# Optimization experiments

Hardware: AMD Instinct MI355X
Metric: run time of the kernel (lower is better)

The kernel has to match this reference:

```python
import jax, jax.numpy as jnp
import numpy as np

B, Q, K, H, V = 16, 128, 512, 256, 256


def setup_inputs() -> dict:
    key = jax.random.key(0)
    ks = jax.random.split(key, 7)
    return {
        "queries": jax.random.normal(ks[0], (B, Q, H), dtype=jnp.float32),
        "keys": jax.random.normal(ks[1], (B, K, H), dtype=jnp.float32),
        "values": jax.random.normal(ks[2], (B, K, V), dtype=jnp.float32),
        "Wq": jax.random.normal(ks[3], (H, H), dtype=jnp.float32) / np.sqrt(H),
        "Wk": jax.random.normal(ks[4], (H, H), dtype=jnp.float32) / np.sqrt(H),
        "Wv": jax.random.normal(ks[5], (H,), dtype=jnp.float32) / np.sqrt(H),
        "valid_lens": jax.random.randint(ks[6], (B,), 1, K + 1, dtype=jnp.int32),
    }


def reference(queries, keys, values, Wq, Wk, Wv, valid_lens):
    # Projections (no bias, matching nn.Linear(..., bias=False))
    q = jnp.einsum("bqd,hd->bqh", queries, Wq)  # W_q: weight is [out,in] in torch; symmetric here
    k = jnp.einsum("bkd,hd->bkh", keys, Wk)
    # Broadcast add -> tanh -> project to scalar score: [B, Q, K]
    features = jnp.tanh(q[:, :, None, :] + k[:, None, :, :])  # [B,Q,K,H]
    scores = jnp.einsum("bqkh,h->bqk", features, Wv)
    # masked_softmax: positions >= valid_len get -1e6 before softmax
    mask = jnp.arange(K)[None, None, :] < valid_lens[:, None, None]  # [B,1,K]
    scores = jnp.where(mask, scores, -1e6)
    attn = jax.nn.softmax(scores, axis=-1)
    # dropout in eval mode = identity
    return jnp.einsum("bqk,bkv->bqv", attn, values)
```

## Files before the change

### kernel.cpp

```cpp
#include <hip/hip_runtime.h>

#define BQ   16
#define QLEN 128
#define KLEN 512
#define HD   256
#define VD   256

typedef __bf16 bf16x8 __attribute__((ext_vector_type(8)));
typedef float  f32x4  __attribute__((ext_vector_type(4)));

static __device__ __forceinline__ float fexp2(float x) {
#if __has_builtin(__builtin_amdgcn_exp2f)
    return __builtin_amdgcn_exp2f(x);
#else
    return exp2f(x);
#endif
}
static __device__ __forceinline__ float frcp(float x) {
#if __has_builtin(__builtin_amdgcn_rcpf)
    return __builtin_amdgcn_rcpf(x);
#else
    return 1.0f / x;
#endif
}

#define EXP_SCALE 2.8853900817779268f

__global__ __launch_bounds__(256) void mfma_proj(
    const float* __restrict__ queries, const float* __restrict__ keys,
    const float* __restrict__ Wq, const float* __restrict__ Wk,
    const int* __restrict__ vlen,
    float* __restrict__ Eq, float* __restrict__ Ekt)
{
    __shared__ __bf16 Ahi_s[64][40];
    __shared__ __bf16 Alo_s[64][40];
    __shared__ __bf16 Whi_s[64][40];
    __shared__ __bf16 Wlo_s[64][40];

    const int t    = threadIdx.x;
    const int ln   = t & 63;
    const int w    = t >> 6;
    const int p    = ln & 15;
    const int quad = ln >> 4;
    const int bx = blockIdx.x, by = blockIdx.y;
    const bool isq = by < 32;
    const int row0 = by * 64;
    const int col0 = bx * 64;

    if (!isq) {
        const int kr0 = row0 - 2048;
        if ((kr0 & 511) >= vlen[kr0 >> 9]) return;
    }

    const float* Ag = isq ? (queries + (size_t)row0 * HD)
                          : (keys + (size_t)(row0 - 2048) * HD);
    const float* Wg = isq ? Wq : Wk;

    const int ar = t >> 2, ac = (t & 3) * 8;

    float4 pa0, pa1, pw0, pw1;
    {
        const float* ap = Ag + ar * HD + ac;
        pa0 = *(const float4*)ap;
        pa1 = *(const float4*)(ap + 4);
        const float* wp = Wg + (size_t)(col0 + ar) * HD + ac;
        pw0 = *(const float4*)wp;
        pw1 = *(const float4*)(wp + 4);
    }

    f32x4 acc[4] = {};

    for (int s = 0; s < 8; ++s) {
        __syncthreads();
        {
            float fa[8] = {pa0.x, pa0.y, pa0.z, pa0.w, pa1.x, pa1.y, pa1.z, pa1.w};
            float fw[8] = {pw0.x, pw0.y, pw0.z, pw0.w, pw1.x, pw1.y, pw1.z, pw1.w};
            bf16x8 ha, la, hw, lw;
            #pragma unroll
            for (int j = 0; j < 8; ++j) {
                __bf16 av = (__bf16)fa[j];
                ha[j] = av;
                la[j] = (__bf16)(fa[j] - (float)av);
                __bf16 wv = (__bf16)fw[j];
                hw[j] = wv;
                lw[j] = (__bf16)(fw[j] - (float)wv);
            }
            *(bf16x8*)&Ahi_s[ar][ac] = ha;
            *(bf16x8*)&Alo_s[ar][ac] = la;
            *(bf16x8*)&Whi_s[ar][ac] = hw;
            *(bf16x8*)&Wlo_s[ar][ac] = lw;
        }
        __syncthreads();
        if (s < 7) {
            const int kc = (s + 1) * 32;
            const float* ap = Ag + ar * HD + kc + ac;
            pa0 = *(const float4*)ap;
            pa1 = *(const float4*)(ap + 4);
            const float* wp = Wg + (size_t)(col0 + ar) * HD + kc + ac;
            pw0 = *(const float4*)wp;
            pw1 = *(const float4*)(wp + 4);
        }
        bf16x8 bh = *(const bf16x8*)&Whi_s[w * 16 + p][quad * 8];
        bf16x8 bl = *(const bf16x8*)&Wlo_s[w * 16 + p][quad * 8];
        #pragma unroll
        for (int mi = 0; mi < 4; ++mi) {
            bf16x8 ah = *(const bf16x8*)&Ahi_s[mi * 16 + p][quad * 8];
            bf16x8 al = *(const bf16x8*)&Alo_s[mi * 16 + p][quad * 8];
            acc[mi] = __builtin_amdgcn_mfma_f32_16x16x32_bf16(ah, bh, acc[mi], 0, 0, 0);
            acc[mi] = __builtin_amdgcn_mfma_f32_16x16x32_bf16(ah, bl, acc[mi], 0, 0, 0);
            acc[mi] = __builtin_amdgcn_mfma_f32_16x16x32_bf16(al, bh, acc[mi], 0, 0, 0);
        }
    }

    #pragma unroll
    for (int mi = 0; mi < 4; ++mi) {
        const int H  = col0 + w * 16 + p;
        const int rl = mi * 16 + quad * 4;
        float e0 = fexp2(acc[mi][0] * EXP_SCALE);
        float e1 = fexp2(acc[mi][1] * EXP_SCALE);
        float e2 = fexp2(acc[mi][2] * EXP_SCALE);
        float e3 = fexp2(acc[mi][3] * EXP_SCALE);
        if (isq) {
            float* dst = Eq + (size_t)(row0 + rl) * HD + H;
            dst[0] = e0; dst[HD] = e1; dst[2 * HD] = e2; dst[3 * HD] = e3;
        } else {
            const int kr = row0 - 2048 + rl;
            const int b = kr >> 9, k0 = kr & 511;
            float4 st; st.x = e0; st.y = e1; st.z = e2; st.w = e3;
            *(float4*)(Ekt + ((size_t)b * HD + H) * KLEN + k0) = st;
        }
    }
}

__global__ __launch_bounds__(256) void proj_exp_gemm(
    const float* __restrict__ Qin, const float* __restrict__ Kin,
    const float* __restrict__ Wq, const float* __restrict__ Wk,
    float* __restrict__ Eq, float* __restrict__ Ekt)
{
    __shared__ union {
        struct { float a[2][16][68]; float w[2][16][68]; } s;
        float tb[64][65];
    } sh;

    const int t  = threadIdx.x;
    const int tx = t & 15, ty = t >> 4;
    const int bx = blockIdx.x, by = blockIdx.y;
    const bool isq = by < 32;
    const int row0 = isq ? by * 64 : (by - 32) * 64;
    const float* A = isq ? Qin : Kin;
    const float* W = isq ? Wq : Wk;
    const int lrow = t >> 2, ld0 = (t & 3) * 4;
    const float* Ab = A + (row0 + lrow) * HD;
    const float* Wb = W + (bx * 64 + lrow) * HD;

    float4 av = *(const float4*)(Ab + ld0);
    float4 wv = *(const float4*)(Wb + ld0);
    sh.s.a[0][ld0 + 0][lrow] = av.x; sh.s.a[0][ld0 + 1][lrow] = av.y;
    sh.s.a[0][ld0 + 2][lrow] = av.z; sh.s.a[0][ld0 + 3][lrow] = av.w;
    sh.s.w[0][ld0 + 0][lrow] = wv.x; sh.s.w[0][ld0 + 1][lrow] = wv.y;
    sh.s.w[0][ld0 + 2][lrow] = wv.z; sh.s.w[0][ld0 + 3][lrow] = wv.w;

    float acc[4][4] = {};
    int p = 0;
    for (int kc = 0; kc < HD; kc += 16) {
        if (kc + 16 < HD) {
            av = *(const float4*)(Ab + kc + 16 + ld0);
            wv = *(const float4*)(Wb + kc + 16 + ld0);
        }
        __syncthreads();
        if (kc + 16 < HD) {
            const int np = p ^ 1;
            sh.s.a[np][ld0 + 0][lrow] = av.x; sh.s.a[np][ld0 + 1][lrow] = av.y;
            sh.s.a[np][ld0 + 2][lrow] = av.z; sh.s.a[np][ld0 + 3][lrow] = av.w;
            sh.s.w[np][ld0 + 0][lrow] = wv.x; sh.s.w[np][ld0 + 1][lrow] = wv.y;
            sh.s.w[np][ld0 + 2][lrow] = wv.z; sh.s.w[np][ld0 + 3][lrow] = wv.w;
        }
        #pragma unroll
        for (int dd = 0; dd < 16; ++dd) {
            float4 a4 = *(const float4*)&sh.s.a[p][dd][ty * 4];
            float4 w4 = *(const float4*)&sh.s.w[p][dd][tx * 4];
            const float* af = (const float*)&a4;
            const float* wf = (const float*)&w4;
            #pragma unroll
            for (int i = 0; i < 4; ++i)
                #pragma unroll
                for (int j = 0; j < 4; ++j)
                    acc[i][j] = fmaf(af[i], wf[j], acc[i][j]);
        }
        p ^= 1;
    }

    float e[4][4];
    #pragma unroll
    for (int i = 0; i < 4; ++i)
        #pragma unroll
        for (int j = 0; j < 4; ++j)
            e[i][j] = fexp2(acc[i][j] * EXP_SCALE);

    if (isq) {
        float* Cb = Eq + (row0 + ty * 4) * HD + bx * 64 + tx * 4;
        #pragma unroll
        for (int i = 0; i < 4; ++i) {
            float4 st; st.x = e[i][0]; st.y = e[i][1]; st.z = e[i][2]; st.w = e[i][3];
            *(float4*)(Cb + i * HD) = st;
        }
    } else {
        __syncthreads();
        #pragma unroll
        for (int j = 0; j < 4; ++j) {
            float4 st; st.x = e[0][j]; st.y = e[1][j]; st.z = e[2][j]; st.w = e[3][j];
            *(float4*)&sh.tb[tx * 4 + j][ty * 4] = st;
        }
        __syncthreads();
        const int r = t >> 2, c0 = (t & 3) * 16;
        const int b = row0 >> 9, kbase = row0 & 511;
        float* dst = Ekt + ((size_t)b * HD + bx * 64 + r) * KLEN + kbase + c0;
        #pragma unroll
        for (int u = 0; u < 4; ++u) {
            float4 v = *(const float4*)&sh.tb[r][c0 + u * 4];
            *(float4*)(dst + u * 4) = v;
        }
    }
}

__global__ __launch_bounds__(512, 4) void fused_attn(
    const float* __restrict__ Eq, const float* __restrict__ Ekt,
    const float* __restrict__ values, const float* __restrict__ Wv,
    const int* __restrict__ vlen, float* __restrict__ out)
{
    __shared__ float eq_s[4][HD];
    __shared__ float wv_s[HD];
    __shared__ float sc[4][KLEN];
    __shared__ float ps[4][4][KLEN];
    __shared__ float wred[4];

    const int t    = threadIdx.x;
    const int b    = blockIdx.x >> 5;
    const int q0   = (blockIdx.x & 31) * 4;
    const int lane = t & 63;
    const int wid  = t >> 6;
    const int len  = vlen[b];
    const bool small = (len <= 256);

    {
        const int h = t & 255, rr = t >> 8;
        eq_s[rr][h]     = Eq[(b * QLEN + q0 + rr) * HD + h];
        eq_s[rr + 2][h] = Eq[(b * QLEN + q0 + rr + 2) * HD + h];
        if (t < HD) {
            float w = Wv[t];
            wv_s[t] = w;
            float ws = w;
            #pragma unroll
            for (int off = 32; off > 0; off >>= 1) ws += __shfl_xor(ws, off, 64);
            if (lane == 0) wred[wid] = ws;
        }
    }
    __syncthreads();
    const float wv_sum = wred[0] + wred[1] + wred[2] + wred[3];

    {
        const int hbase = small ? (wid * 32) : ((wid & 3) * 64);
        const int hcnt  = small ? 32 : 64;
        const int kload = small ? (lane * 4) : ((wid >> 2) * 256 + lane * 4);
        const int col   = (wid >> 2) * 256 + lane * 4;
        const float* ek = Ekt + ((size_t)b * HD + hbase) * KLEN + kload;
        float acc[4] = {};
        float accb[4] = {};
        float4 n0 = *(const float4*)(ek + 0 * KLEN);
        float4 n1 = *(const float4*)(ek + 1 * KLEN);
        float4 n2 = *(const float4*)(ek + 2 * KLEN);
        float4 n3 = *(const float4*)(ek + 3 * KLEN);
        float acc2[4][4] = {};
        for (int hh = 0; hh < hcnt; hh += 4) {
            float4 e0 = n0, e1 = n1, e2 = n2, e3 = n3;
            if (hh + 4 < hcnt) {
                const float* nk = ek + (size_t)(hh + 4) * KLEN;
                n0 = *(const float4*)(nk + 0 * KLEN);
                n1 = *(const float4*)(nk + 1 * KLEN);
                n2 = *(const float4*)(nk + 2 * KLEN);
                n3 = *(const float4*)(nk + 3 * KLEN);
            }
            const float* E0 = (const float*)&e0;
            const float* E1 = (const float*)&e1;
            const float* E2 = (const float*)&e2;
            const float* E3 = (const float*)&e3;
            const float w0 = wv_s[hbase + hh + 0], w1 = wv_s[hbase + hh + 1];
            const float w2 = wv_s[hbase + hh + 2], w3 = wv_s[hbase + hh + 3];
            #pragma unroll
            for (int i = 0; i < 4; ++i) {
                const float a0 = eq_s[i][hbase + hh + 0], a1 = eq_s[i][hbase + hh + 1];
                const float a2 = eq_s[i][hbase + hh + 2], a3 = eq_s[i][hbase + hh + 3];
                #pragma unroll
                for (int j = 0; j < 4; ++j) {
                    float d0 = fmaf(a0, E0[j], 1.f);
                    float d1 = fmaf(a1, E1[j], 1.f);
                    float d2 = fmaf(a2, E2[j], 1.f);
                    float d3 = fmaf(a3, E3[j], 1.f);
                    float d01 = d0 * d1, d23 = d2 * d3;
                    float n01 = fmaf(w1, d0, w0 * d1);
                    float n23 = fmaf(w3, d2, w2 * d3);
                    float top = fmaf(n23, d01, n01 * d23);
                    acc2[i][j] = fmaf(top, frcp(d01 * d23), acc2[i][j]);
                }
            }
        }
        (void)acc; (void)accb;
        #pragma unroll
        for (int i = 0; i < 4; ++i) {
            float4 st; st.x = acc2[i][0]; st.y = acc2[i][1]; st.z = acc2[i][2]; st.w = acc2[i][3];
            *(float4*)&ps[wid & 3][i][col] = st;
        }
    }
    __syncthreads();

    if (wid < 4) {
        float s[8];
        float m = -3.0e38f;
        if (small) {
            #pragma unroll
            for (int j = 0; j < 4; ++j) {
                int k = lane + j * 64;
                float raw = ps[0][wid][k] + ps[1][wid][k] + ps[2][wid][k] + ps[3][wid][k]
                          + ps[0][wid][k + 256] + ps[1][wid][k + 256]
                          + ps[2][wid][k + 256] + ps[3][wid][k + 256];
                float v = fmaf(-2.f, raw, wv_sum);
                v = (k < len) ? v : -1.0e6f;
                s[j] = v;
                m = fmaxf(m, v);
            }
            #pragma unroll
            for (int j = 4; j < 8; ++j) s[j] = -1.0e6f;
        } else {
            #pragma unroll
            for (int j = 0; j < 8; ++j) {
                int k = lane + j * 64;
                float raw = ps[0][wid][k] + ps[1][wid][k] + ps[2][wid][k] + ps[3][wid][k];
                float v = fmaf(-2.f, raw, wv_sum);
                v = (k < len) ? v : -1.0e6f;
                s[j] = v;
                m = fmaxf(m, v);
            }
        }
        #pragma unroll
        for (int off = 32; off > 0; off >>= 1) m = fmaxf(m, __shfl_xor(m, off, 64));
        float sum = 0.f;
        #pragma unroll
        for (int j = 0; j < 8; ++j) {
            float ev = fexp2(1.4426950408889634f * (s[j] - m));
            s[j] = ev;
            sum += ev;
        }
        #pragma unroll
        for (int off = 32; off > 0; off >>= 1) sum += __shfl_xor(sum, off, 64);
        const float rs = frcp(sum);
        const int jmax = small ? 4 : 8;
        for (int j = 0; j < jmax; ++j) sc[wid][lane + j * 64] = s[j] * rs;
    }
    __syncthreads();

    float (*po)[4][VD] = (float (*)[4][VD])ps;
    const int kq = wid & 3, vh = wid >> 2;
    const int kk = lane >> 5, vv = lane & 31;
    const int v0 = vh * 128 + vv * 4;
    const int kbase = small ? kq * 64 : kq * 128;
    const int kcnt  = small ? 64 : 128;
    {
        const float* vb = values + (size_t)b * KLEN * VD + (size_t)(kbase + kk) * VD + v0;
        float o[4][4] = {};
        for (int ks = 0; ks < kcnt; ks += 2) {
            const int k = kbase + ks + kk;
            float4 v4 = *(const float4*)(vb + (size_t)ks * VD);
            float p0 = sc[0][k], p1 = sc[1][k], p2 = sc[2][k], p3 = sc[3][k];
            o[0][0] = fmaf(p0, v4.x, o[0][0]); o[0][1] = fmaf(p0, v4.y, o[0][1]);
            o[0][2] = fmaf(p0, v4.z, o[0][2]); o[0][3] = fmaf(p0, v4.w, o[0][3]);
            o[1][0] = fmaf(p1, v4.x, o[1][0]); o[1][1] = fmaf(p1, v4.y, o[1][1]);
            o[1][2] = fmaf(p1, v4.z, o[1][2]); o[1][3] = fmaf(p1, v4.w, o[1][3]);
            o[2][0] = fmaf(p2, v4.x, o[2][0]); o[2][1] = fmaf(p2, v4.y, o[2][1]);
            o[2][2] = fmaf(p2, v4.z, o[2][2]); o[2][3] = fmaf(p2, v4.w, o[2][3]);
            o[3][0] = fmaf(p3, v4.x, o[3][0]); o[3][1] = fmaf(p3, v4.y, o[3][1]);
            o[3][2] = fmaf(p3, v4.z, o[3][2]); o[3][3] = fmaf(p3, v4.w, o[3][3]);
        }
        __syncthreads();
        #pragma unroll
        for (int r = 0; r < 4; ++r) {
            #pragma unroll
            for (int c = 0; c < 4; ++c) o[r][c] += __shfl_xor(o[r][c], 32, 64);
        }
        if (kk == 0) {
            #pragma unroll
            for (int r = 0; r < 4; ++r) {
                float4 st; st.x = o[r][0]; st.y = o[r][1]; st.z = o[r][2]; st.w = o[r][3];
                *(float4*)&po[kq][r][v0] = st;
            }
        }
    }
    __syncthreads();

    #pragma unroll
    for (int u = 0; u < 2; ++u) {
        int idx = t + u * 512;
        int r = idx >> 8, c = idx & 255;
        out[(b * QLEN + q0 + r) * VD + c] =
            po[0][r][c] + po[1][r][c] + po[2][r][c] + po[3][r][c];
    }
}

extern "C" void kernel_launch(void* const* d_in, const int* in_sizes, int n_in,
                              void* d_out, int out_size, void* d_ws, size_t ws_size,
                              hipStream_t stream) {
    const float* queries = (const float*)d_in[0];
    const float* keys    = (const float*)d_in[1];
    const float* values  = (const float*)d_in[2];
    const float* Wq      = (const float*)d_in[3];
    const float* Wk      = (const float*)d_in[4];
    const float* Wv      = (const float*)d_in[5];
    const int*   vl      = (const int*)d_in[6];
    float* out = (float*)d_out;

    float* Eq  = (float*)d_ws;
    float* Ekt = Eq + 2048 * 256;

    if (ws_size >= 10485760) {
        mfma_proj<<<dim3(4, 160), 256, 0, stream>>>(queries, keys, Wq, Wk, vl, Eq, Ekt);
    } else {
        proj_exp_gemm<<<dim3(4, 160), 256, 0, stream>>>(queries, keys, Wq, Wk, Eq, Ekt);
    }
    fused_attn<<<dim3(512), 512, 0, stream>>>(Eq, Ekt, values, Wv, vl, out);
}
```

Baseline: 132.2 us.

## Template score loop, deepen prefetch, and bound PV loop by valid length

```diff
diff --git a/kernel.cpp b/kernel.cpp
--- a/kernel.cpp
+++ b/kernel.cpp
@@ -223,6 +223,61 @@
     }
 }
 
+template<int HCNT>
+static __device__ __forceinline__ void score_slice(
+    const float* __restrict__ ek, int hbase,
+    const float (* __restrict__ eq_s)[HD], const float* __restrict__ wv_s,
+    float acc[4][4])
+{
+    float4 pa0 = *(const float4*)(ek + 0 * KLEN);
+    float4 pa1 = *(const float4*)(ek + 1 * KLEN);
+    float4 pa2 = *(const float4*)(ek + 2 * KLEN);
+    float4 pa3 = *(const float4*)(ek + 3 * KLEN);
+    float4 pb0 = pa0, pb1 = pa1, pb2 = pa2, pb3 = pa3;
+    if (HCNT > 4) {
+        const float* p = ek + (size_t)4 * KLEN;
+        pb0 = *(const float4*)(p);
+        pb1 = *(const float4*)(p + KLEN);
+        pb2 = *(const float4*)(p + 2 * KLEN);
+        pb3 = *(const float4*)(p + 3 * KLEN);
+    }
+    #pragma unroll
+    for (int hh = 0; hh < HCNT; hh += 4) {
+        float4 e0 = pa0, e1 = pa1, e2 = pa2, e3 = pa3;
+        pa0 = pb0; pa1 = pb1; pa2 = pb2; pa3 = pb3;
+        if (hh + 8 < HCNT) {
+            const float* p = ek + (size_t)(hh + 8) * KLEN;
+            pb0 = *(const float4*)(p);
+            pb1 = *(const float4*)(p + KLEN);
+            pb2 = *(const float4*)(p + 2 * KLEN);
+            pb3 = *(const float4*)(p + 3 * KLEN);
+        }
+        const float* E0 = (const float*)&e0;
+        const float* E1 = (const float*)&e1;
+        const float* E2 = (const float*)&e2;
+        const float* E3 = (const float*)&e3;
+        const float w0 = wv_s[hbase + hh + 0], w1 = wv_s[hbase + hh + 1];
+        const float w2 = wv_s[hbase + hh + 2], w3 = wv_s[hbase + hh + 3];
+        #pragma unroll
+        for (int i = 0; i < 4; ++i) {
+            const float a0 = eq_s[i][hbase + hh + 0], a1 = eq_s[i][hbase + hh + 1];
+            const float a2 = eq_s[i][hbase + hh + 2], a3 = eq_s[i][hbase + hh + 3];
+            #pragma unroll
+            for (int j = 0; j < 4; ++j) {
+                float d0 = fmaf(a0, E0[j], 1.f);
+                float d1 = fmaf(a1, E1[j], 1.f);
+                float d2 = fmaf(a2, E2[j], 1.f);
+                float d3 = fmaf(a3, E3[j], 1.f);
+                float d01 = d0 * d1, d23 = d2 * d3;
+                float n01 = fmaf(w1, d0, w0 * d1);
+                float n23 = fmaf(w3, d2, w2 * d3);
+                float top = fmaf(n23, d01, n01 * d23);
+                acc[i][j] = fmaf(top, frcp(d01 * d23), acc[i][j]);
+            }
+        }
+    }
+}
+
 __global__ __launch_bounds__(512, 4) void fused_attn(
     const float* __restrict__ Eq, const float* __restrict__ Ekt,
     const float* __restrict__ values, const float* __restrict__ Wv,
@@ -258,57 +313,29 @@
     __syncthreads();
     const float wv_sum = wred[0] + wred[1] + wred[2] + wred[3];
 
-    {
-        const int hbase = small ? (wid * 32) : ((wid & 3) * 64);
-        const int hcnt  = small ? 32 : 64;
-        const int kload = small ? (lane * 4) : ((wid >> 2) * 256 + lane * 4);
-        const int col   = (wid >> 2) * 256 + lane * 4;
-        const float* ek = Ekt + ((size_t)b * HD + hbase) * KLEN + kload;
-        float acc[4] = {};
-        float accb[4] = {};
-        float4 n0 = *(const float4*)(ek + 0 * KLEN);
-        float4 n1 = *(const float4*)(ek + 1 * KLEN);
-        float4 n2 = *(const float4*)(ek + 2 * KLEN);
-        float4 n3 = *(const float4*)(ek + 3 * KLEN);
-        float acc2[4][4] = {};
-        for (int hh = 0; hh < hcnt; hh += 4) {
-            float4 e0 = n0, e1 = n1, e2 = n2, e3 = n3;
-            if (hh + 4 < hcnt) {
-                const float* nk = ek + (size_t)(hh + 4) * KLEN;
-                n0 = *(const float4*)(nk + 0 * KLEN);
-                n1 = *(const float4*)(nk + 1 * KLEN);
-                n2 = *(const float4*)(nk + 2 * KLEN);
-                n3 = *(const float4*)(nk + 3 * KLEN);
-            }
-            const float* E0 = (const float*)&e0;
-            const float* E1 = (const float*)&e1;
-            const float* E2 = (const float*)&e2;
-            const float* E3 = (const float*)&e3;
-            const float w0 = wv_s[hbase + hh + 0], w1 = wv_s[hbase + hh + 1];
-            const float w2 = wv_s[hbase + hh + 2], w3 = wv_s[hbase + hh + 3];
-            #pragma unroll
-            for (int i = 0; i < 4; ++i) {
-                const float a0 = eq_s[i][hbase + hh + 0], a1 = eq_s[i][hbase + hh + 1];
-                const float a2 = eq_s[i][hbase + hh + 2], a3 = eq_s[i][hbase + hh + 3];
-                #pragma unroll
-                for (int j = 0; j < 4; ++j) {
-                    float d0 = fmaf(a0, E0[j], 1.f);
-                    float d1 = fmaf(a1, E1[j], 1.f);
-                    float d2 = fmaf(a2, E2[j], 1.f);
-                    float d3 = fmaf(a3, E3[j], 1.f);
-                    float d01 = d0 * d1, d23 = d2 * d3;
-                    float n01 = fmaf(w1, d0, w0 * d1);
-                    float n23 = fmaf(w3, d2, w2 * d3);
-                    float top = fmaf(n23, d01, n01 * d23);
-                    acc2[i][j] = fmaf(top, frcp(d01 * d23), acc2[i][j]);
-                }
-            }
-        }
-        (void)acc; (void)accb;
+    float (*ps8)[4][256] = (float (*)[4][256])ps;
+
+    if (small) {
+        const int hbase = wid * 32;
+        const int k4    = lane * 4;
+        const float* ek = Ekt + ((size_t)b * HD + hbase) * KLEN + k4;
+        float acc[4][4] = {};
+        score_slice<32>(ek, hbase, eq_s, wv_s, acc);
         #pragma unroll
         for (int i = 0; i < 4; ++i) {
-            float4 st; st.x = acc2[i][0]; st.y = acc2[i][1]; st.z = acc2[i][2]; st.w = acc2[i][3];
-            *(float4*)&ps[wid & 3][i][col] = st;
+            float4 st; st.x = acc[i][0]; st.y = acc[i][1]; st.z = acc[i][2]; st.w = acc[i][3];
+            *(float4*)&ps8[wid][i][k4] = st;
+        }
+    } else {
+        const int hbase = (wid & 3) * 64;
+        const int k4    = (wid >> 2) * 256 + lane * 4;
+        const float* ek = Ekt + ((size_t)b * HD + hbase) * KLEN + k4;
+        float acc[4][4] = {};
+        score_slice<64>(ek, hbase, eq_s, wv_s, acc);
+        #pragma unroll
+        for (int i = 0; i < 4; ++i) {
+            float4 st; st.x = acc[i][0]; st.y = acc[i][1]; st.z = acc[i][2]; st.w = acc[i][3];
+            *(float4*)&ps[wid & 3][i][k4] = st;
         }
     }
     __syncthreads();
@@ -320,9 +347,8 @@
             #pragma unroll
             for (int j = 0; j < 4; ++j) {
                 int k = lane + j * 64;
-                float raw = ps[0][wid][k] + ps[1][wid][k] + ps[2][wid][k] + ps[3][wid][k]
-                          + ps[0][wid][k + 256] + ps[1][wid][k + 256]
-                          + ps[2][wid][k + 256] + ps[3][wid][k + 256];
+                float raw = ps8[0][wid][k] + ps8[1][wid][k] + ps8[2][wid][k] + ps8[3][wid][k]
+                          + ps8[4][wid][k] + ps8[5][wid][k] + ps8[6][wid][k] + ps8[7][wid][k];
                 float v = fmaf(-2.f, raw, wv_sum);
                 v = (k < len) ? v : -1.0e6f;
                 s[j] = v;
@@ -359,15 +385,15 @@
     __syncthreads();
 
     float (*po)[4][VD] = (float (*)[4][VD])ps;
+    const int Cr4 = ((len + 7) >> 3) << 1;
     const int kq = wid & 3, vh = wid >> 2;
     const int kk = lane >> 5, vv = lane & 31;
     const int v0 = vh * 128 + vv * 4;
-    const int kbase = small ? kq * 64 : kq * 128;
-    const int kcnt  = small ? 64 : 128;
+    const int kbase = kq * Cr4;
     {
         const float* vb = values + (size_t)b * KLEN * VD + (size_t)(kbase + kk) * VD + v0;
         float o[4][4] = {};
-        for (int ks = 0; ks < kcnt; ks += 2) {
+        for (int ks = 0; ks < Cr4; ks += 2) {
             const int k = kbase + ks + kk;
             float4 v4 = *(const float4*)(vb + (size_t)ks * VD);
             float p0 = sc[0][k], p1 = sc[1][k], p2 = sc[2][k], p3 = sc[3][k];
```

Result: slower. 487.0 us (+268.5%).
